# Kernel optimization log

Hardware: AMD Instinct MI355X
Metric: run time of the kernel (lower is better)

The kernel has to match this reference:

```python
import jax, jax.numpy as jnp
import numpy as np

MAX_DEPTH = 6
NUM_TREES = 64
LEAF_DIMS = 128
D_IN = 512
BATCH = 4096
N_INTERNAL = 2 ** MAX_DEPTH - 1  # 63
N_LEAVES = 2 ** MAX_DEPTH        # 64


def setup_inputs() -> dict:
    key = jax.random.key(0)
    ks = jax.random.split(key, 4)
    x = jax.random.normal(ks[0], (BATCH, D_IN), dtype=jnp.float32)
    # Stacked internal-node dense layers, node i at index i (level order, node_index ordering)
    W = jax.random.normal(ks[1], (N_INTERNAL, D_IN, NUM_TREES), dtype=jnp.float32) / np.sqrt(D_IN)
    b = jnp.zeros((N_INTERNAL, NUM_TREES), dtype=jnp.float32)
    leaf_weight = jax.random.normal(ks[2], (N_LEAVES, LEAF_DIMS, NUM_TREES), dtype=jnp.float32)
    gates = jax.random.normal(ks[3], (N_LEAVES, LEAF_DIMS, NUM_TREES), dtype=jnp.float32)
    return {"x": x, "W": W, "b": b, "leaf_weight": leaf_weight, "gates": gates}


def reference(x, W, b, leaf_weight, gates):
    # All internal-node gating probabilities in one batched matmul:
    # g[b, n, t] = sigmoid(x[b] @ W[n] + b[n])  for every internal node n, tree t
    g = jax.nn.sigmoid(jnp.einsum('bd,ndt->bnt', x, W) + b[None, :, :])  # [B, 63, T]

    B = x.shape[0]
    T = W.shape[-1]
    # Path probability to each leaf, built level by level.
    # Level l has 2^l nodes at internal indices [2^l - 1, 2^(l+1) - 2];
    # interleaving (left=p*g, right=p*(1-g)) matches node_index child ordering.
    p = jnp.ones((B, 1, T), dtype=x.dtype)
    for level in range(MAX_DEPTH):
        start = 2 ** level - 1
        n_lvl = 2 ** level
        gl = g[:, start:start + n_lvl, :]                  # [B, n_lvl, T]
        children = jnp.stack([p * gl, p * (1.0 - gl)], axis=2)  # [B, n_lvl, 2, T]
        p = children.reshape(B, 2 * n_lvl, T)
    # p: [B, n_leaves, T] leaf path probabilities

    # Softmax mixture-of-experts gate over trees, then weighted leaf mixture:
    # out[b, d] = sum_{l, t} p[b, l, t] * leaf_weight[l, d, t] * softmax(gates, -1)[l, d, t]
    w = leaf_weight * jax.nn.softmax(gates, axis=-1)  # [L, D, T]
    out = jnp.einsum('blt,ldt->bd', p, w)
    return out
```

## Files before the change

kernel.cpp:

```cpp
#include <hip/hip_runtime.h>
#include <stdint.h>

#define BATCH 4096
#define DIN   512
#define NT    64
#define NL    64
#define LD    128

typedef __attribute__((ext_vector_type(8))) short bf16x8;
typedef __attribute__((ext_vector_type(8))) _Float16 f16x8;
typedef __attribute__((ext_vector_type(4))) float f32x4;

typedef const __attribute__((address_space(1))) unsigned char* gcp_t;
typedef __attribute__((address_space(3))) unsigned char* lp_t;

__device__ __forceinline__ void gl_lds16(const void* g, void* l) {
  __builtin_amdgcn_global_load_lds((gcp_t)g, (lp_t)l, 16, 0, 0);
}

__device__ __forceinline__ unsigned short f2bf(float f) {
  union { float f; unsigned u; } a; a.f = f;
  unsigned r = a.u + 0x7FFFu + ((a.u >> 16) & 1u);
  return (unsigned short)(r >> 16);
}

__global__ __launch_bounds__(256) void prep_all_k(
    const float* __restrict__ x, const float* __restrict__ W,
    const float* __restrict__ gates, const float* __restrict__ lw,
    unsigned short* __restrict__ xb, unsigned short* __restrict__ Wt,
    unsigned short* __restrict__ Wv2) {
  __shared__ float smem[12288];
  const int bx = blockIdx.x;
  const int tid = threadIdx.x;

  if (bx < 2048) {
    int i = bx * 256 + tid;
    float4 v = ((const float4*)x)[i];
    ushort4 o;
    o.x = f2bf(v.x); o.y = f2bf(v.y); o.z = f2bf(v.z); o.w = f2bf(v.w);
    ((ushort4*)xb)[i] = o;
  } else if (bx < 2304) {
    int bb = bx - 2048;
    int n = bb >> 2, d0 = (bb & 3) * 128;
    float* buf = smem;
    if (n < 63) {
      for (int it = 0; it < 32; ++it) {
        int idx = it * 256 + tid;
        buf[idx] = W[n * 32768 + (d0 + (idx >> 6)) * 64 + (idx & 63)];
      }
    }
    __syncthreads();
    int t = tid >> 2, q = tid & 3;
    unsigned short vals[32];
    #pragma unroll
    for (int j = 0; j < 32; ++j)
      vals[j] = (n < 63) ? f2bf(buf[(q * 32 + j) * 64 + t]) : (unsigned short)0;
    uint4* dst = (uint4*)(Wt + t * 32768 + n * 512 + d0 + q * 32);
    const uint4* src = (const uint4*)vals;
    dst[0] = src[0]; dst[1] = src[1]; dst[2] = src[2]; dst[3] = src[3];
  } else {
    int d = bx - 2304;
    float* gb = smem;
    float* lb = smem + 4096;
    float* wv = smem + 8192;
    for (int it = 0; it < 16; ++it) {
      int idx = it * 256 + tid;
      int l = idx >> 6;
      int ga = l * 8192 + d * 64 + (idx & 63);
      gb[idx] = gates[ga];
      lb[idx] = lw[ga];
    }
    __syncthreads();
    int wave = tid >> 6, lane = tid & 63;
    for (int l = wave; l < 64; l += 4) {
      float v = gb[l * 64 + lane];
      float mx = v;
      for (int m = 32; m >= 1; m >>= 1) mx = fmaxf(mx, __shfl_xor(mx, m));
      float e = __expf(v - mx);
      float s = e;
      for (int m = 32; m >= 1; m >>= 1) s += __shfl_xor(s, m);
      wv[l * 64 + lane] = lb[l * 64 + lane] * e / s;
    }
    __syncthreads();
    #pragma unroll
    for (int c = 0; c < 2; ++c) {
      int k0 = tid * 16 + c * 8;
      union { unsigned short u[8]; uint4 v; } o;
      #pragma unroll
      for (int j = 0; j < 8; ++j) {
        int k = k0 + j;
        o.u[j] = f2bf(wv[(k & 63) * 64 + (k >> 6)]);
      }
      *(uint4*)(Wv2 + (long)d * 4096 + k0) = o.v;
    }
  }
}

__global__ __launch_bounds__(256, 3) void gemm1_tree_k(
    const unsigned short* __restrict__ xb,
    const unsigned short* __restrict__ Wt,
    const float* __restrict__ bias,
    unsigned short* __restrict__ P)
{
  __shared__ unsigned short As[128 * 32];
  __shared__ unsigned short Bs[128 * 32];
  __shared__ __align__(16) _Float16 gbuf[128 * 136];
  __shared__ float bb[128];

  const int tid = threadIdx.x;
  const int wave = tid >> 6, lane = tid & 63;
  const int b0 = blockIdx.x * 128;
  const int t0 = blockIdx.y * 2;

  if (tid < 128) {
    int n = tid & 63, t = t0 + (tid >> 6);
    bb[tid] = (n < 63) ? bias[n * 64 + t] : 0.0f;
  }

  const f32x4 zero = {0.f, 0.f, 0.f, 0.f};
  f32x4 acc[4][4];
  #pragma unroll
  for (int i = 0; i < 4; ++i)
    #pragma unroll
    for (int j = 0; j < 4; ++j) acc[i][j] = zero;

  const int g0 = wave * 64 + lane;
  const int g1 = g0 + 256;
  const unsigned short* Ag0 = xb + (long)(b0 + (g0 >> 2)) * 512 + (g0 & 3) * 8;
  const unsigned short* Ag1 = xb + (long)(b0 + (g1 >> 2)) * 512 + (g1 & 3) * 8;
  const unsigned short* Bg0 = Wt + (long)(t0 * 64 + (g0 >> 2)) * 512 + (g0 & 3) * 8;
  const unsigned short* Bg1 = Wt + (long)(t0 * 64 + (g1 >> 2)) * 512 + (g1 & 3) * 8;
  unsigned short* lA0 = As + (wave * 64) * 8;
  unsigned short* lA1 = As + (wave * 64 + 256) * 8;
  unsigned short* lB0 = Bs + (wave * 64) * 8;
  unsigned short* lB1 = Bs + (wave * 64 + 256) * 8;

  const int wm = (wave >> 1) * 64, wn = (wave & 1) * 64;
  const int mrow = lane & 15, kg = lane >> 4;

  for (int kk = 0; kk < 512; kk += 32) {
    __syncthreads();
    gl_lds16(Ag0 + kk, lA0);
    gl_lds16(Ag1 + kk, lA1);
    gl_lds16(Bg0 + kk, lB0);
    gl_lds16(Bg1 + kk, lB1);
    asm volatile("s_waitcnt vmcnt(0)" ::: "memory");
    __syncthreads();

    bf16x8 fa[4], fb[4];
    #pragma unroll
    for (int i = 0; i < 4; ++i)
      fa[i] = *(const bf16x8*)(As + (wm + i * 16 + mrow) * 32 + kg * 8);
    #pragma unroll
    for (int j = 0; j < 4; ++j)
      fb[j] = *(const bf16x8*)(Bs + (wn + j * 16 + mrow) * 32 + kg * 8);
    #pragma unroll
    for (int i = 0; i < 4; ++i)
      #pragma unroll
      for (int j = 0; j < 4; ++j)
        acc[i][j] = __builtin_amdgcn_mfma_f32_16x16x32_bf16(fa[i], fb[j], acc[i][j], 0, 0, 0);
  }

  #pragma unroll
  for (int i = 0; i < 4; ++i)
    #pragma unroll
    for (int j = 0; j < 4; ++j) {
      int col = wn + j * 16 + mrow;
      float bv = bb[col];
      #pragma unroll
      for (int r = 0; r < 4; ++r) {
        int row = wm + i * 16 + kg * 4 + r;
        float z = acc[i][j][r] + bv;
        gbuf[row * 136 + col] = (_Float16)(1.0f / (1.0f + __expf(-z)));
      }
    }
  __syncthreads();

  {
    const int row = tid >> 1, tr = tid & 1;
    const _Float16* grow = gbuf + row * 136 + tr * 64;
    float g[63];
    #pragma unroll
    for (int c = 0; c < 8; ++c) {
      f16x8 gv = *(const f16x8*)(grow + c * 8);
      #pragma unroll
      for (int j = 0; j < 8; ++j) {
        int n = c * 8 + j;
        if (n < 63) g[n] = (float)gv[j];
      }
    }
    float P3[8];
    {
      float a0 = g[0],            a1 = 1.0f - g[0];
      float c0 = a0 * g[1],       c1 = a0 * (1.0f - g[1]);
      float c2 = a1 * g[2],       c3 = a1 * (1.0f - g[2]);
      P3[0] = c0 * g[3];  P3[1] = c0 * (1.0f - g[3]);
      P3[2] = c1 * g[4];  P3[3] = c1 * (1.0f - g[4]);
      P3[4] = c2 * g[5];  P3[5] = c2 * (1.0f - g[5]);
      P3[6] = c3 * g[6];  P3[7] = c3 * (1.0f - g[6]);
    }
    unsigned short* prow = P + (long)(b0 + row) * 4096 + (t0 + tr) * 64;
    #pragma unroll
    for (int o = 0; o < 8; ++o) {
      float g3 = g[7 + o];
      float q0 = P3[o] * g3, q1 = P3[o] * (1.0f - g3);
      float g4a = g[15 + 2 * o], g4b = g[16 + 2 * o];
      float r0 = q0 * g4a, r1 = q0 * (1.0f - g4a);
      float r2 = q1 * g4b, r3 = q1 * (1.0f - g4b);
      union { unsigned short u[8]; uint4 v; } ou;
      #pragma unroll
      for (int h = 0; h < 4; ++h) {
        float g5 = g[31 + 4 * o + h];
        float rr = (h == 0) ? r0 : (h == 1) ? r1 : (h == 2) ? r2 : r3;
        ou.u[2 * h]     = f2bf(rr * g5);
        ou.u[2 * h + 1] = f2bf(rr * (1.0f - g5));
      }
      *(uint4*)(prow + o * 8) = ou.v;
    }
  }
}

__global__ __launch_bounds__(256, 4) void gemm2_k(
    const unsigned short* __restrict__ P,
    const unsigned short* __restrict__ Wv2,
    float* __restrict__ out)
{
  __shared__ unsigned short As[64 * 32];
  __shared__ unsigned short Bs[128 * 32];
  const int tid = threadIdx.x;
  const int wave = tid >> 6, lane = tid & 63;
  const int b0 = blockIdx.x * 64;
  const int kc = blockIdx.y;

  const f32x4 zero = {0.f, 0.f, 0.f, 0.f};
  f32x4 acc[2][4];
  #pragma unroll
  for (int i = 0; i < 2; ++i)
    #pragma unroll
    for (int j = 0; j < 4; ++j) acc[i][j] = zero;

  const int g0 = wave * 64 + lane;
  const int g1 = g0 + 256;
  const unsigned short* Ag0 = P + (long)(b0 + (g0 >> 2)) * 4096 + kc * 512 + (g0 & 3) * 8;
  const unsigned short* Bg0 = Wv2 + (long)(g0 >> 2) * 4096 + kc * 512 + (g0 & 3) * 8;
  const unsigned short* Bg1 = Wv2 + (long)(g1 >> 2) * 4096 + kc * 512 + (g1 & 3) * 8;
  unsigned short* lA0 = As + (wave * 64) * 8;
  unsigned short* lB0 = Bs + (wave * 64) * 8;
  unsigned short* lB1 = Bs + (wave * 64 + 256) * 8;

  const int wm = (wave >> 1) * 32, wn = (wave & 1) * 64;
  const int mrow = lane & 15, kg = lane >> 4;

  for (int kk = 0; kk < 512; kk += 32) {
    __syncthreads();
    gl_lds16(Ag0 + kk, lA0);
    gl_lds16(Bg0 + kk, lB0);
    gl_lds16(Bg1 + kk, lB1);
    asm volatile("s_waitcnt vmcnt(0)" ::: "memory");
    __syncthreads();

    bf16x8 fa[2], fb[4];
    #pragma unroll
    for (int i = 0; i < 2; ++i)
      fa[i] = *(const bf16x8*)(As + (wm + i * 16 + mrow) * 32 + kg * 8);
    #pragma unroll
    for (int j = 0; j < 4; ++j)
      fb[j] = *(const bf16x8*)(Bs + (wn + j * 16 + mrow) * 32 + kg * 8);
    #pragma unroll
    for (int i = 0; i < 2; ++i)
      #pragma unroll
      for (int j = 0; j < 4; ++j)
        acc[i][j] = __builtin_amdgcn_mfma_f32_16x16x32_bf16(fa[i], fb[j], acc[i][j], 0, 0, 0);
  }

  #pragma unroll
  for (int i = 0; i < 2; ++i)
    #pragma unroll
    for (int j = 0; j < 4; ++j) {
      int col = wn + j * 16 + mrow;
      #pragma unroll
      for (int r = 0; r < 4; ++r) {
        int row = wm + i * 16 + kg * 4 + r;
        atomicAdd(&out[(long)(b0 + row) * 128 + col], acc[i][j][r]);
      }
    }
}

extern "C" void kernel_launch(void* const* d_in, const int* in_sizes, int n_in,
                              void* d_out, int out_size, void* d_ws, size_t ws_size,
                              hipStream_t stream) {
  const float* x     = (const float*)d_in[0];
  const float* W     = (const float*)d_in[1];
  const float* b     = (const float*)d_in[2];
  const float* lw    = (const float*)d_in[3];
  const float* gates = (const float*)d_in[4];
  float* out = (float*)d_out;

  char* ws = (char*)d_ws;
  unsigned short* xb  = (unsigned short*)(ws);
  unsigned short* Wt  = (unsigned short*)(ws + (4l  << 20));
  unsigned short* Wv2 = (unsigned short*)(ws + (8l  << 20));
  unsigned short* P   = (unsigned short*)(ws + (16l << 20));

  hipMemsetAsync(out, 0, (size_t)4096 * 128 * sizeof(float), stream);
  hipLaunchKernelGGL(prep_all_k,   dim3(2432),   dim3(256), 0, stream,
                     x, W, gates, lw, xb, Wt, Wv2);
  hipLaunchKernelGGL(gemm1_tree_k, dim3(32, 32), dim3(256), 0, stream, xb, Wt, b, P);
  hipLaunchKernelGGL(gemm2_k,      dim3(64, 8),  dim3(256), 0, stream, P, Wv2, out);
}
```

Before: 147.8 us.

## Double-buffer LDS loads in both GEMMs and split gemm2 K across more blocks

Both GEMM kernels now prefetch the next K-slice into a second LDS buffer while MFMAs consume the current one. Partial vmcnt waits and raw barriers replace the full load-then-sync pattern. gemm1 reuses the staging buffers for its sigmoid tile (gbuf aliased onto smem) to stay within an occupancy of 4. gemm2 splits K into 16 chunks of 256, doubling the grid to expose more parallelism, at the cost of twice as many fp32 atomic adds into the output.

New measurement: 154.5 us. 1.05x slower.

```diff
diff --git a/kernel.cpp b/kernel.cpp
--- a/kernel.cpp
+++ b/kernel.cpp
@@ -96,16 +96,17 @@
   }
 }
 
-__global__ __launch_bounds__(256, 3) void gemm1_tree_k(
+__global__ __launch_bounds__(256, 4) void gemm1_tree_k(
     const unsigned short* __restrict__ xb,
     const unsigned short* __restrict__ Wt,
     const float* __restrict__ bias,
     unsigned short* __restrict__ P)
 {
-  __shared__ unsigned short As[128 * 32];
-  __shared__ unsigned short Bs[128 * 32];
-  __shared__ __align__(16) _Float16 gbuf[128 * 136];
+  __shared__ __align__(16) char smem[34816];
   __shared__ float bb[128];
+  unsigned short* AsB = (unsigned short*)smem;
+  unsigned short* BsB = (unsigned short*)(smem + 16384);
+  _Float16* gbuf = (_Float16*)smem;
 
   const int tid = threadIdx.x;
   const int wave = tid >> 6, lane = tid & 63;
@@ -130,35 +131,47 @@
   const unsigned short* Ag1 = xb + (long)(b0 + (g1 >> 2)) * 512 + (g1 & 3) * 8;
   const unsigned short* Bg0 = Wt + (long)(t0 * 64 + (g0 >> 2)) * 512 + (g0 & 3) * 8;
   const unsigned short* Bg1 = Wt + (long)(t0 * 64 + (g1 >> 2)) * 512 + (g1 & 3) * 8;
-  unsigned short* lA0 = As + (wave * 64) * 8;
-  unsigned short* lA1 = As + (wave * 64 + 256) * 8;
-  unsigned short* lB0 = Bs + (wave * 64) * 8;
-  unsigned short* lB1 = Bs + (wave * 64 + 256) * 8;
+  const int lofs0 = wave * 512;
+  const int lofs1 = wave * 512 + 2048;
 
   const int wm = (wave >> 1) * 64, wn = (wave & 1) * 64;
   const int mrow = lane & 15, kg = lane >> 4;
 
-  for (int kk = 0; kk < 512; kk += 32) {
-    __syncthreads();
-    gl_lds16(Ag0 + kk, lA0);
-    gl_lds16(Ag1 + kk, lA1);
-    gl_lds16(Bg0 + kk, lB0);
-    gl_lds16(Bg1 + kk, lB1);
-    asm volatile("s_waitcnt vmcnt(0)" ::: "memory");
-    __syncthreads();
+  gl_lds16(Ag0, AsB + lofs0);
+  gl_lds16(Ag1, AsB + lofs1);
+  gl_lds16(Bg0, BsB + lofs0);
+  gl_lds16(Bg1, BsB + lofs1);
+
+  for (int it = 0; it < 16; ++it) {
+    const int buf = (it & 1) * 4096;
+    if (it < 15) {
+      const int kk = (it + 1) * 32;
+      const int nbuf = ((it + 1) & 1) * 4096;
+      gl_lds16(Ag0 + kk, AsB + nbuf + lofs0);
+      gl_lds16(Ag1 + kk, AsB + nbuf + lofs1);
+      gl_lds16(Bg0 + kk, BsB + nbuf + lofs0);
+      gl_lds16(Bg1 + kk, BsB + nbuf + lofs1);
+      asm volatile("s_waitcnt vmcnt(4)" ::: "memory");
+    } else {
+      asm volatile("s_waitcnt vmcnt(0)" ::: "memory");
+    }
+    asm volatile("s_barrier" ::: "memory");
 
     bf16x8 fa[4], fb[4];
     #pragma unroll
     for (int i = 0; i < 4; ++i)
-      fa[i] = *(const bf16x8*)(As + (wm + i * 16 + mrow) * 32 + kg * 8);
+      fa[i] = *(const bf16x8*)(AsB + buf + (wm + i * 16 + mrow) * 32 + kg * 8);
     #pragma unroll
     for (int j = 0; j < 4; ++j)
-      fb[j] = *(const bf16x8*)(Bs + (wn + j * 16 + mrow) * 32 + kg * 8);
+      fb[j] = *(const bf16x8*)(BsB + buf + (wn + j * 16 + mrow) * 32 + kg * 8);
     #pragma unroll
     for (int i = 0; i < 4; ++i)
       #pragma unroll
       for (int j = 0; j < 4; ++j)
         acc[i][j] = __builtin_amdgcn_mfma_f32_16x16x32_bf16(fa[i], fb[j], acc[i][j], 0, 0, 0);
+
+    asm volatile("s_waitcnt lgkmcnt(0)" ::: "memory");
+    asm volatile("s_barrier" ::: "memory");
   }
 
   #pragma unroll
@@ -225,12 +238,12 @@
     const unsigned short* __restrict__ Wv2,
     float* __restrict__ out)
 {
-  __shared__ unsigned short As[64 * 32];
-  __shared__ unsigned short Bs[128 * 32];
+  __shared__ unsigned short AsB[2][64 * 32];
+  __shared__ unsigned short BsB[2][128 * 32];
   const int tid = threadIdx.x;
   const int wave = tid >> 6, lane = tid & 63;
   const int b0 = blockIdx.x * 64;
-  const int kc = blockIdx.y;
+  const int k0 = blockIdx.y * 256;
 
   const f32x4 zero = {0.f, 0.f, 0.f, 0.f};
   f32x4 acc[2][4];
@@ -241,36 +254,47 @@
 
   const int g0 = wave * 64 + lane;
   const int g1 = g0 + 256;
-  const unsigned short* Ag0 = P + (long)(b0 + (g0 >> 2)) * 4096 + kc * 512 + (g0 & 3) * 8;
-  const unsigned short* Bg0 = Wv2 + (long)(g0 >> 2) * 4096 + kc * 512 + (g0 & 3) * 8;
-  const unsigned short* Bg1 = Wv2 + (long)(g1 >> 2) * 4096 + kc * 512 + (g1 & 3) * 8;
-  unsigned short* lA0 = As + (wave * 64) * 8;
-  unsigned short* lB0 = Bs + (wave * 64) * 8;
-  unsigned short* lB1 = Bs + (wave * 64 + 256) * 8;
+  const unsigned short* Ag0 = P + (long)(b0 + (g0 >> 2)) * 4096 + k0 + (g0 & 3) * 8;
+  const unsigned short* Bg0 = Wv2 + (long)(g0 >> 2) * 4096 + k0 + (g0 & 3) * 8;
+  const unsigned short* Bg1 = Wv2 + (long)(g1 >> 2) * 4096 + k0 + (g1 & 3) * 8;
+  const int lofs = wave * 512;
 
   const int wm = (wave >> 1) * 32, wn = (wave & 1) * 64;
   const int mrow = lane & 15, kg = lane >> 4;
 
-  for (int kk = 0; kk < 512; kk += 32) {
-    __syncthreads();
-    gl_lds16(Ag0 + kk, lA0);
-    gl_lds16(Bg0 + kk, lB0);
-    gl_lds16(Bg1 + kk, lB1);
-    asm volatile("s_waitcnt vmcnt(0)" ::: "memory");
-    __syncthreads();
+  gl_lds16(Ag0, AsB[0] + lofs);
+  gl_lds16(Bg0, BsB[0] + lofs);
+  gl_lds16(Bg1, BsB[0] + lofs + 2048);
+
+  for (int it = 0; it < 8; ++it) {
+    const int buf = it & 1;
+    if (it < 7) {
+      const int kk = (it + 1) * 32;
+      const int nbuf = (it + 1) & 1;
+      gl_lds16(Ag0 + kk, AsB[nbuf] + lofs);
+      gl_lds16(Bg0 + kk, BsB[nbuf] + lofs);
+      gl_lds16(Bg1 + kk, BsB[nbuf] + lofs + 2048);
+      asm volatile("s_waitcnt vmcnt(3)" ::: "memory");
+    } else {
+      asm volatile("s_waitcnt vmcnt(0)" ::: "memory");
+    }
+    asm volatile("s_barrier" ::: "memory");
 
     bf16x8 fa[2], fb[4];
     #pragma unroll
     for (int i = 0; i < 2; ++i)
-      fa[i] = *(const bf16x8*)(As + (wm + i * 16 + mrow) * 32 + kg * 8);
+      fa[i] = *(const bf16x8*)(AsB[buf] + (wm + i * 16 + mrow) * 32 + kg * 8);
     #pragma unroll
     for (int j = 0; j < 4; ++j)
-      fb[j] = *(const bf16x8*)(Bs + (wn + j * 16 + mrow) * 32 + kg * 8);
+      fb[j] = *(const bf16x8*)(BsB[buf] + (wn + j * 16 + mrow) * 32 + kg * 8);
     #pragma unroll
     for (int i = 0; i < 2; ++i)
       #pragma unroll
       for (int j = 0; j < 4; ++j)
         acc[i][j] = __builtin_amdgcn_mfma_f32_16x16x32_bf16(fa[i], fb[j], acc[i][j], 0, 0, 0);
+
+    asm volatile("s_waitcnt lgkmcnt(0)" ::: "memory");
+    asm volatile("s_barrier" ::: "memory");
   }
 
   #pragma unroll
@@ -306,5 +330,5 @@
   hipLaunchKernelGGL(prep_all_k,   dim3(2432),   dim3(256), 0, stream,
                      x, W, gates, lw, xb, Wt, Wv2);
   hipLaunchKernelGGL(gemm1_tree_k, dim3(32, 32), dim3(256), 0, stream, xb, Wt, b, P);
-  hipLaunchKernelGGL(gemm2_k,      dim3(64, 8),  dim3(256), 0, stream, P, Wv2, out);
-}
+  hipLaunchKernelGGL(gemm2_k,      dim3(64, 16), dim3(256), 0, stream, P, Wv2, out);
+}
```
